# Kernel tuning notes

Measured on AMD Instinct MI355X. Metric: run time of the kernel, lower is better.

The kernel has to match this reference:

```python
import jax, jax.numpy as jnp
import numpy as np

NX, NU, N, BATCH = 64, 32, 32, 192
NEWTON_ITERS = 2  # fixed outer Newton iterations (original loops to kkt_tol)


def setup_inputs() -> dict:
    key = jax.random.key(0)
    ks = jax.random.split(key, 8)
    x0 = jax.random.normal(ks[0], (BATCH, NX), jnp.float32)
    x = 0.1 * jax.random.normal(ks[1], (N + 1, BATCH, NX), jnp.float32)
    u = 0.1 * jax.random.normal(ks[2], (N, BATCH, NU), jnp.float32)
    lmd = jnp.zeros((N + 1, BATCH, NX), jnp.float32)
    # linear dynamics x+ = A x + Bm u (stable-ish A)
    A = 0.9 * jnp.eye(NX, dtype=jnp.float32) + (0.1 / np.sqrt(NX)) * jax.random.normal(ks[3], (NX, NX), jnp.float32)
    Bm = jax.random.normal(ks[4], (NX, NU), jnp.float32) / np.sqrt(NX)
    # quadratic cost weights (symmetric PD)
    Cx = jax.random.normal(ks[5], (NX, NX), jnp.float32) / np.sqrt(NX)
    Qx = Cx @ Cx.T + 0.1 * jnp.eye(NX, dtype=jnp.float32)
    Cu = jax.random.normal(ks[6], (NU, NU), jnp.float32) / np.sqrt(NU)
    Ru = Cu @ Cu.T + jnp.eye(NU, dtype=jnp.float32)
    Cf = jax.random.normal(ks[7], (NX, NX), jnp.float32) / np.sqrt(NX)
    Qf = Cf @ Cf.T + 0.1 * jnp.eye(NX, dtype=jnp.float32)
    return {"x0": x0, "x": x, "u": u, "lmd": lmd, "A": A, "Bm": Bm, "Qx": Qx, "Ru": Ru, "Qf": Qf}


def _eval_kkt(x0, x, u, lmd, A, Bm, Qx, Ru, Qf):
    # KKT residuals of the LQ OCP (GaussNewton; vectorized over stages s and batch b)
    x0res = x[0] - x0                                                   # [B,nx]
    xs = x[:-1]                                                         # [N,B,nx]
    xres = jnp.einsum('ij,sbj->sbi', A, xs) + jnp.einsum('ij,sbj->sbi', Bm, u) - x[1:]
    lx = jnp.einsum('ij,sbj->sbi', Qx, xs) + jnp.einsum('ji,sbj->sbi', A, lmd[1:]) - lmd[:-1]
    lu = jnp.einsum('ij,sbj->sbi', Ru, u) + jnp.einsum('ji,sbj->sbi', Bm, lmd[1:])
    lxN = jnp.einsum('ij,bj->bi', Qf, x[-1]) - lmd[-1]                  # terminal gradient residual
    return x0res, xres, lx, lu, lxN


def _riccati(x0res, xres, lx, lu, lxN, A, Bm, Qx, Ru, Qf):
    B_, nx = x0res.shape
    PN = jnp.broadcast_to(Qf, (B_, nx, nx))

    def bwd(carry, inp):
        P, p = carry
        lx_i, lu_i, xres_i = inp
        PA = jnp.einsum('bij,jk->bik', P, A)
        PB = jnp.einsum('bij,jk->bik', P, Bm)
        Qxx = Qx[None] + jnp.einsum('ji,bjk->bik', A, PA)
        Quu = Ru[None] + jnp.einsum('ji,bjk->bik', Bm, PB)
        Qxu = jnp.einsum('ji,bjk->bik', A, PB)
        w = jnp.einsum('bij,bj->bi', P, xres_i) + p
        qx = lx_i + jnp.einsum('ji,bj->bi', A, w)
        qu = lu_i + jnp.einsum('ji,bj->bi', Bm, w)
        rhs = jnp.concatenate([jnp.swapaxes(Qxu, 1, 2), qu[..., None]], axis=2)
        sol = -jnp.linalg.solve(Quu, rhs)
        K, k = sol[..., :nx], sol[..., nx]
        Pn = Qxx + jnp.einsum('bxi,biy->bxy', Qxu, K)
        Pn = 0.5 * (Pn + jnp.swapaxes(Pn, 1, 2))
        pn = qx + jnp.einsum('bxi,bi->bx', Qxu, k)
        return (Pn, pn), (Pn, pn, K, k)

    (_, _), (Ps, ps, Ks, ks) = jax.lax.scan(bwd, (PN, lxN), (lx, lu, xres), reverse=True)
    Ps = jnp.concatenate([Ps, PN[None]], axis=0)   # [N+1,B,nx,nx]
    ps = jnp.concatenate([ps, lxN[None]], axis=0)  # [N+1,B,nx]

    def fwd(dx, inp):
        K, k, xres_i = inp
        du = jnp.einsum('bux,bx->bu', K, dx) + k
        dxn = jnp.einsum('ij,bj->bi', A, dx) + jnp.einsum('ij,bj->bi', Bm, du) + xres_i
        return dxn, (dx, du)

    dxN, (dxs, dus) = jax.lax.scan(fwd, -x0res, (Ks, ks, xres))
    dxs = jnp.concatenate([dxs, dxN[None]], axis=0)
    dlmd = jnp.einsum('sbij,sbj->sbi', Ps, dxs) + ps
    return dxs, dus, dlmd


def _solve(x0, x, u, lmd, A, Bm, Qx, Ru, Qf):
    for _ in range(NEWTON_ITERS):
        x0res, xres, lx, lu, lxN = _eval_kkt(x0, x, u, lmd, A, Bm, Qx, Ru, Qf)
        dx, du, dlmd = _riccati(x0res, xres, lx, lu, lxN, A, Bm, Qx, Ru, Qf)
        x = x + dx
        u = u + du
        lmd = lmd + dlmd
    return x, u, lmd


def reference(x0, x, u, lmd, A, Bm, Qx, Ru, Qf):
    # returns the optimized control trajectory u* [N,B,nu]
    return _solve(x0, x, u, lmd, A, Bm, Qx, Ru, Qf)[1]
```

## Files before the change

kernel.cpp:

```cpp
#include <hip/hip_runtime.h>

#define DEV __device__ __forceinline__

constexpr int NX = 64, NU = 32, NH = 32, NB = 192;

constexpr int WS_P  = 0;
constexpr int WS_QI = WS_P  + (NH + 1) * NX * NX;
constexpr int WS_XT = WS_QI + NH * NU * NU;
constexpr int WS_K  = WS_XT + NH * NU * NX;

typedef __attribute__((ext_vector_type(8))) short bf16x8;
typedef __attribute__((ext_vector_type(4))) float f32x4;
typedef __attribute__((ext_vector_type(4))) unsigned short us4;

constexpr int oM2Th = 0;
constexpr int oM2Tl = 13824;
constexpr int oPh   = 27648;
constexpr int oPl   = 36864;
constexpr int oTTh  = 46080;
constexpr int oTTl  = 59904;
constexpr int oXUh  = 73728;
constexpr int oXUl  = 78848;
constexpr int oKTh  = 83968;
constexpr int oKTl  = 89088;
constexpr int oQIh  = 94208;
constexpr int oQIl  = 96768;
constexpr int oQXX  = 99328;
constexpr int oQUU  = 116736;
constexpr int SMEMB = 121344;

DEV unsigned short bfh(float x) {
  unsigned u = __float_as_uint(x);
  return (unsigned short)((u + 0x7FFFu + ((u >> 16) & 1u)) >> 16);
}
DEV float bf2f(unsigned short h) { return __uint_as_float(((unsigned)h) << 16); }
DEV bf16x8 ldf(const char* base, int byteoff) { return *(const bf16x8*)(base + byteoff); }
DEV void st_pack4(char* hb, char* lb, int elemoff, f32x4 v) {
  us4 h, l;
#pragma unroll
  for (int r = 0; r < 4; ++r) {
    unsigned short hh = bfh(v[r]);
    h[r] = (short)hh;
    l[r] = (short)bfh(v[r] - bf2f(hh));
  }
  *(us4*)(hb + elemoff * 2) = h;
  *(us4*)(lb + elemoff * 2) = l;
}

DEV float4 ld4(const float* p) { return *reinterpret_cast<const float4*>(p); }
DEV void   st4(float* p, float4 v) { *reinterpret_cast<float4*>(p) = v; }
DEV float  dot4(float4 a, float4 b) {
  return fmaf(a.x, b.x, fmaf(a.y, b.y, fmaf(a.z, b.z, a.w * b.w)));
}
DEV void fma4(float4& a, float s, float4 b) {
  a.x = fmaf(s, b.x, a.x); a.y = fmaf(s, b.y, a.y);
  a.z = fmaf(s, b.z, a.z); a.w = fmaf(s, b.w, a.w);
}
DEV void fma8(float* acc, float s, float4 b0, float4 b1) {
  acc[0] = fmaf(s, b0.x, acc[0]); acc[1] = fmaf(s, b0.y, acc[1]);
  acc[2] = fmaf(s, b0.z, acc[2]); acc[3] = fmaf(s, b0.w, acc[3]);
  acc[4] = fmaf(s, b1.x, acc[4]); acc[5] = fmaf(s, b1.y, acc[5]);
  acc[6] = fmaf(s, b1.z, acc[6]); acc[7] = fmaf(s, b1.w, acc[7]);
}

#define MFMA16(a, b, c) __builtin_amdgcn_mfma_f32_16x16x32_bf16(a, b, c, 0, 0, 0)

DEV void producer(char* smem, const float* Ag, const float* Bg,
                  const float* Qxg, const float* Rug, const float* Qfg,
                  float* ws) {
  const int t = threadIdx.x, lane = t & 63, wv = t >> 6;
  const int l15 = lane & 15, l4 = lane >> 4;

  char* M2Th = smem + oM2Th; char* M2Tl = smem + oM2Tl;
  char* Ph   = smem + oPh;   char* Pl   = smem + oPl;
  char* TTh  = smem + oTTh;  char* TTl  = smem + oTTl;
  char* XUh  = smem + oXUh;  char* XUl  = smem + oXUl;
  char* KTh  = smem + oKTh;  char* KTl  = smem + oKTl;
  char* QIh  = smem + oQIh;  char* QIl  = smem + oQIl;
  float* QXX = (float*)(smem + oQXX);
  float* QUU = (float*)(smem + oQUU);

  float* gP  = ws + WS_P;
  float* gQI = ws + WS_QI;
  float* gXT = ws + WS_XT;
  float* gK  = ws + WS_K;
  int* flags = (int*)(ws + WS_P);

  for (int idx = t; idx < 96 * 64; idx += 512) {
    const int j = idx >> 6, m = idx & 63;
    const float v = (j < 64) ? Ag[m * 64 + j] : Bg[m * 32 + (j - 64)];
    const unsigned short h = bfh(v);
    *(unsigned short*)(M2Th + (j * 72 + m) * 2) = h;
    *(unsigned short*)(M2Tl + (j * 72 + m) * 2) = bfh(v - bf2f(h));
  }
  for (int idx = t; idx < 64 * 64; idx += 512) {
    const int r = idx >> 6, c = idx & 63;
    const float v = Qfg[idx];
    const unsigned short h = bfh(v);
    *(unsigned short*)(Ph + (r * 72 + c) * 2) = h;
    *(unsigned short*)(Pl + (r * 72 + c) * 2) = bfh(v - bf2f(h));
    gP[32 * 4096 + idx] = v;
  }
  __syncthreads();

  for (int s = NH - 1; s >= 0; --s) {
    for (int tt = wv; tt < 24; tt += 8) {
      const int mT = tt & 3, jT = tt >> 2;
      f32x4 acc = {0.f, 0.f, 0.f, 0.f};
#pragma unroll
      for (int kp = 0; kp < 2; ++kp) {
        const int ko = (kp * 32 + l4 * 8) * 2;
        const bf16x8 ah = ldf(Ph,   (mT * 16 + l15) * 144 + ko);
        const bf16x8 al = ldf(Pl,   (mT * 16 + l15) * 144 + ko);
        const bf16x8 bh = ldf(M2Th, (jT * 16 + l15) * 144 + ko);
        const bf16x8 bl = ldf(M2Tl, (jT * 16 + l15) * 144 + ko);
        acc = MFMA16(ah, bh, acc);
        acc = MFMA16(ah, bl, acc);
        acc = MFMA16(al, bh, acc);
      }
      st_pack4(TTh, TTl, (jT * 16 + l15) * 72 + mT * 16 + l4 * 4, acc);
    }
    __syncthreads();

    for (int tt = wv; tt < 36; tt += 8) {
      const int jT = tt / 6, iT = tt % 6;
      f32x4 acc = {0.f, 0.f, 0.f, 0.f};
#pragma unroll
      for (int kp = 0; kp < 2; ++kp) {
        const int ko = (kp * 32 + l4 * 8) * 2;
        const bf16x8 ah = ldf(TTh,  (jT * 16 + l15) * 144 + ko);
        const bf16x8 al = ldf(TTl,  (jT * 16 + l15) * 144 + ko);
        const bf16x8 bh = ldf(M2Th, (iT * 16 + l15) * 144 + ko);
        const bf16x8 bl = ldf(M2Tl, (iT * 16 + l15) * 144 + ko);
        acc = MFMA16(ah, bh, acc);
        acc = MFMA16(ah, bl, acc);
        acc = MFMA16(al, bh, acc);
      }
      const int c = iT * 16 + l15;
      const int j0 = jT * 16 + l4 * 4;
      if (jT < 4 && iT < 4) {
        const float4 q = ld4(Qxg + c * 64 + j0);
        float4 o; o.x = acc[0] + q.x; o.y = acc[1] + q.y;
        o.z = acc[2] + q.z; o.w = acc[3] + q.w;
        st4(QXX + c * 68 + j0, o);
      } else if (jT < 4) {
        const int n = c - 64;
        float4 o; o.x = acc[0]; o.y = acc[1]; o.z = acc[2]; o.w = acc[3];
        st4(gXT + s * 2048 + n * 64 + j0, o);
      } else if (iT < 4) {
        st_pack4(XUh, XUl, c * 40 + (j0 - 64), acc);
      } else {
        const int b = c - 64, a0 = j0 - 64;
        const float4 rv = ld4(Rug + b * 32 + a0);
        float4 o; o.x = acc[0] + rv.x; o.y = acc[1] + rv.y;
        o.z = acc[2] + rv.z; o.w = acc[3] + rv.w;
        st4(QUU + b * 36 + a0, o);
      }
    }
    __syncthreads();

    if (wv == 0) {
      const int i = lane & 31, h = lane >> 5;
      float W[16];
#pragma unroll
      for (int r = 0; r < 16; ++r) W[r] = QUU[i * 36 + h * 16 + r];
#pragma unroll
      for (int j = 0; j < 32; ++j) {
        const int jh = j >> 4, jr = j & 15;
        const float d = __shfl(W[jr], j | (jh << 5));
        const float pinv = 1.0f / d;
        const float f = __shfl(W[jr], i | (jh << 5));
        float pr[16];
#pragma unroll
        for (int r = 0; r < 16; ++r) pr[r] = __shfl(W[r], j | (h << 5));
        float nw[16];
        if (i == j) {
#pragma unroll
          for (int r = 0; r < 16; ++r) nw[r] = pr[r] * pinv;
          if (h == jh) nw[jr] = pinv;
        } else {
          const float g = f * pinv;
#pragma unroll
          for (int r = 0; r < 16; ++r) nw[r] = fmaf(-g, pr[r], W[r]);
          if (h == jh) nw[jr] = -g;
        }
#pragma unroll
        for (int r = 0; r < 16; ++r) W[r] = nw[r];
      }
#pragma unroll
      for (int q = 0; q < 4; ++q) {
        float4 o; o.x = W[4 * q]; o.y = W[4 * q + 1];
        o.z = W[4 * q + 2]; o.w = W[4 * q + 3];
        st4(gQI + s * 1024 + i * 32 + h * 16 + 4 * q, o);
        us4 hh, ll;
#pragma unroll
        for (int r = 0; r < 4; ++r) {
          const unsigned short hv = bfh(W[4 * q + r]);
          hh[r] = (short)hv;
          ll[r] = (short)bfh(W[4 * q + r] - bf2f(hv));
        }
        *(us4*)(QIh + (i * 40 + h * 16 + 4 * q) * 2) = hh;
        *(us4*)(QIl + (i * 40 + h * 16 + 4 * q) * 2) = ll;
      }
    }
    __syncthreads();

    {
      const int mT = wv & 1, xT = wv >> 1;
      f32x4 acc = {0.f, 0.f, 0.f, 0.f};
      const int ko = (l4 * 8) * 2;
      const bf16x8 ah = ldf(QIh, (mT * 16 + l15) * 80 + ko);
      const bf16x8 al = ldf(QIl, (mT * 16 + l15) * 80 + ko);
      const bf16x8 bh = ldf(XUh, (xT * 16 + l15) * 80 + ko);
      const bf16x8 bl = ldf(XUl, (xT * 16 + l15) * 80 + ko);
      acc = MFMA16(ah, bh, acc);
      acc = MFMA16(ah, bl, acc);
      acc = MFMA16(al, bh, acc);
      const int x = xT * 16 + l15, m0 = mT * 16 + l4 * 4;
#pragma unroll
      for (int r = 0; r < 4; ++r) gK[s * 2048 + (m0 + r) * 64 + x] = -acc[r];
      st_pack4(KTh, KTl, x * 40 + m0, acc);
    }
    __syncthreads();

    if (t == 0) {
      __threadfence();
      __hip_atomic_store(flags + s, 1, __ATOMIC_RELEASE, __HIP_MEMORY_SCOPE_AGENT);
    }

    if (s > 0) {
      for (int tt = wv; tt < 16; tt += 8) {
        const int iT = tt & 3, jT = tt >> 2;
        f32x4 acc = {0.f, 0.f, 0.f, 0.f};
        const int ko = (l4 * 8) * 2;
        const bf16x8 ah = ldf(XUh, (iT * 16 + l15) * 80 + ko);
        const bf16x8 al = ldf(XUl, (iT * 16 + l15) * 80 + ko);
        const bf16x8 bh = ldf(KTh, (jT * 16 + l15) * 80 + ko);
        const bf16x8 bl = ldf(KTl, (jT * 16 + l15) * 80 + ko);
        acc = MFMA16(ah, bh, acc);
        acc = MFMA16(ah, bl, acc);
        acc = MFMA16(al, bh, acc);
        const int j = jT * 16 + l15, i0 = iT * 16 + l4 * 4;
        f32x4 pv;
#pragma unroll
        for (int r = 0; r < 4; ++r) {
          pv[r] = QXX[(i0 + r) * 68 + j] - acc[r];
          gP[s * 4096 + (i0 + r) * 64 + j] = pv[r];
        }
        st_pack4(Ph, Pl, j * 72 + i0, pv);
      }
    }
    __syncthreads();
  }
}

DEV void consumer(float* lds, int b, const float* x0g, const float* xg,
                  const float* ug, const float* lg, const float* Ag,
                  const float* Bg, const float* Qxg, const float* Rug,
                  const float* Qfg, float* ws, float* outp) {
  const int t = threadIdx.x;
  const float* gP  = ws + WS_P;
  const float* gQI = ws + WS_QI;
  const float* gXT = ws + WS_XT;
  const float* gK  = ws + WS_K;
  const int* flags = (const int*)(ws + WS_P);

  float* sx   = lds;
  float* sl   = lds + 2112;
  float* su   = lds + 4224;
  float* sAT  = lds;
  float* xres = lds + 5248;
  float* lxs  = lds + 7296;
  float* lus  = lds + 9344;
  float* kv   = lds + 10368;
  float* swv  = lds + 11392;
  float* sqv  = lds + 11456;
  float* sduv = lds + 11488;
  float* sdxv = lds + 11520;

  for (int idx = t; idx < (NH + 1) * NX; idx += 512) {
    const int s = idx >> 6, i = idx & 63;
    sx[idx] = xg[(s * NB + b) * NX + i];
    sl[idx] = lg[(s * NB + b) * NX + i];
  }
  for (int idx = t; idx < NH * NU; idx += 512) {
    const int s = idx >> 5, j = idx & 31;
    su[idx] = ug[(s * NB + b) * NU + j];
  }
  __syncthreads();

  if (t < 256) {
    const int s = t >> 3, i0 = (t & 7) * 8;
    float accx[8], accl[8];
#pragma unroll
    for (int ii = 0; ii < 8; ++ii) {
      accx[ii] = -sx[(s + 1) * NX + i0 + ii];
      accl[ii] = -sl[s * NX + i0 + ii];
    }
#pragma unroll 2
    for (int k0 = 0; k0 < NX; k0 += 4) {
      const float4 xv = ld4(sx + s * NX + k0);
#pragma unroll
      for (int ii = 0; ii < 8; ++ii) {
        accx[ii] += dot4(ld4(Ag + (i0 + ii) * NX + k0), xv);
        accl[ii] += dot4(ld4(Qxg + (i0 + ii) * NX + k0), xv);
      }
    }
#pragma unroll 2
    for (int k0 = 0; k0 < NU; k0 += 4) {
      const float4 uv = ld4(su + s * NU + k0);
#pragma unroll
      for (int ii = 0; ii < 8; ++ii)
        accx[ii] += dot4(ld4(Bg + (i0 + ii) * NU + k0), uv);
    }
#pragma unroll 4
    for (int k = 0; k < NX; ++k) {
      const float lv = sl[(s + 1) * NX + k];
      fma8(accl, lv, ld4(Ag + k * NX + i0), ld4(Ag + k * NX + i0 + 4));
    }
#pragma unroll
    for (int ii = 0; ii < 8; ++ii) {
      xres[s * NX + i0 + ii] = accx[ii];
      lxs[s * NX + i0 + ii] = accl[ii];
    }
  }
  if (t < 256) {
    const int s = t >> 3, j0 = (t & 7) * 4;
    float4 acc = {0, 0, 0, 0};
#pragma unroll 2
    for (int k0 = 0; k0 < NU; k0 += 4) {
      const float4 uv = ld4(su + s * NU + k0);
      acc.x += dot4(ld4(Rug + (j0 + 0) * NU + k0), uv);
      acc.y += dot4(ld4(Rug + (j0 + 1) * NU + k0), uv);
      acc.z += dot4(ld4(Rug + (j0 + 2) * NU + k0), uv);
      acc.w += dot4(ld4(Rug + (j0 + 3) * NU + k0), uv);
    }
#pragma unroll 4
    for (int k = 0; k < NX; ++k) {
      const float lv = sl[(s + 1) * NX + k];
      fma4(acc, lv, ld4(Bg + k * NU + j0));
    }
    lus[s * NU + j0 + 0] = acc.x; lus[s * NU + j0 + 1] = acc.y;
    lus[s * NU + j0 + 2] = acc.z; lus[s * NU + j0 + 3] = acc.w;
  }

  float p_i = 0.0f, dx_i = 0.0f;
  if (t < 64) {
    const int i = t;
    float acc = -sl[NH * NX + i];
#pragma unroll 4
    for (int k0 = 0; k0 < NX; k0 += 4)
      acc += dot4(ld4(Qfg + i * NX + k0), ld4(sx + NH * NX + k0));
    p_i = acc;
    dx_i = x0g[b * NX + i] - sx[i];
  }
  __syncthreads();

  for (int idx = t; idx < NX * NX / 4; idx += 512) {
    const int k = idx >> 4, i4 = (idx & 15) * 4;
    const float4 a4 = ld4(Ag + k * NX + i4);
    sAT[(i4 + 0) * 68 + k] = a4.x;
    sAT[(i4 + 1) * 68 + k] = a4.y;
    sAT[(i4 + 2) * 68 + k] = a4.z;
    sAT[(i4 + 3) * 68 + k] = a4.w;
  }
  __syncthreads();

  if (t >= 64) return;

  const int i = t;
  const int j = t & 31;
  const int hh = t >> 5;

  for (int s = NH - 1; s >= 0; --s) {
    while (__hip_atomic_load(flags + s, __ATOMIC_ACQUIRE, __HIP_MEMORY_SCOPE_AGENT) == 0)
      __builtin_amdgcn_s_sleep(16);

    const float* Pr = gP + (s + 1) * NX * NX + i * NX;
    const float* xr = xres + s * NX;
    float w = p_i;
#pragma unroll
    for (int k0 = 0; k0 < NX; k0 += 16) {
      w += dot4(ld4(Pr + k0),      ld4(xr + k0));
      w += dot4(ld4(Pr + k0 + 4),  ld4(xr + k0 + 4));
      w += dot4(ld4(Pr + k0 + 8),  ld4(xr + k0 + 8));
      w += dot4(ld4(Pr + k0 + 12), ld4(xr + k0 + 12));
    }
    swv[i] = w;

    float qx = lxs[s * NX + i];
#pragma unroll
    for (int k0 = 0; k0 < NX; k0 += 16) {
      qx += dot4(ld4(sAT + i * 68 + k0),      ld4(swv + k0));
      qx += dot4(ld4(sAT + i * 68 + k0 + 4),  ld4(swv + k0 + 4));
      qx += dot4(ld4(sAT + i * 68 + k0 + 8),  ld4(swv + k0 + 8));
      qx += dot4(ld4(sAT + i * 68 + k0 + 12), ld4(swv + k0 + 12));
    }

    float qa = 0.0f;
    const int kb = hh * 32;
#pragma unroll 8
    for (int kk = 0; kk < 32; ++kk)
      qa = fmaf(Bg[(kb + kk) * NU + j], swv[kb + kk], qa);
    qa += __shfl_xor(qa, 32);
    const float qu = qa + lus[s * NU + j];
    if (hh == 0) sqv[j] = qu;

    const float* Qr = gQI + s * NU * NU + j * NU + hh * 16;
    float ka = dot4(ld4(Qr),      ld4(sqv + hh * 16))
             + dot4(ld4(Qr + 4),  ld4(sqv + hh * 16 + 4))
             + dot4(ld4(Qr + 8),  ld4(sqv + hh * 16 + 8))
             + dot4(ld4(Qr + 12), ld4(sqv + hh * 16 + 12));
    ka += __shfl_xor(ka, 32);
    if (hh == 0) kv[s * NU + j] = -ka;

    const float* Xs = gXT + s * NU * NX;
    float pp = qx;
#pragma unroll 8
    for (int m = 0; m < NU; ++m)
      pp = fmaf(Xs[m * NX + i], kv[s * NU + m], pp);
    p_i = pp;
  }

  sdxv[i] = dx_i;
  for (int s = 0; s < NH; ++s) {
    const float* Kr = gK + s * NU * NX + j * NX + hh * 32;
    const float* dxh = sdxv + hh * 32;
    float da = 0.0f;
#pragma unroll
    for (int k0 = 0; k0 < 32; k0 += 16) {
      da += dot4(ld4(Kr + k0),      ld4(dxh + k0));
      da += dot4(ld4(Kr + k0 + 4),  ld4(dxh + k0 + 4));
      da += dot4(ld4(Kr + k0 + 8),  ld4(dxh + k0 + 8));
      da += dot4(ld4(Kr + k0 + 12), ld4(dxh + k0 + 12));
    }
    da += __shfl_xor(da, 32);
    const float du = da + kv[s * NU + j];
    if (hh == 0) {
      const int gi = (s * NB + b) * NU + j;
      outp[gi] = ug[gi] + du;
      sduv[j] = du;
    }

    float nxv = xres[s * NX + i];
    const float* Ar = Ag + i * NX;
#pragma unroll
    for (int k0 = 0; k0 < NX; k0 += 4)
      nxv += dot4(ld4(Ar + k0), ld4(sdxv + k0));
    const float* Br = Bg + i * NU;
#pragma unroll
    for (int m0 = 0; m0 < NU; m0 += 4)
      nxv += dot4(ld4(Br + m0), ld4(sduv + m0));
    sdxv[i] = nxv;
  }
}

__global__ void k_zero(float* ws) {
  if (threadIdx.x < 64) ((int*)(ws + WS_P))[threadIdx.x] = 0;
}

__global__ __launch_bounds__(512) void k_fused(
    const float* __restrict__ x0g, const float* __restrict__ xg,
    const float* __restrict__ ug, const float* __restrict__ lg,
    const float* __restrict__ Ag, const float* __restrict__ Bg,
    const float* __restrict__ Qxg, const float* __restrict__ Rug,
    const float* __restrict__ Qfg, float* __restrict__ ws,
    float* __restrict__ outp) {
  __shared__ __align__(16) char smem[SMEMB];
  if (blockIdx.x == 0)
    producer(smem, Ag, Bg, Qxg, Rug, Qfg, ws);
  else
    consumer((float*)smem, blockIdx.x - 1, x0g, xg, ug, lg, Ag, Bg, Qxg, Rug,
             Qfg, ws, outp);
}

extern "C" void kernel_launch(void* const* d_in, const int* in_sizes, int n_in,
                              void* d_out, int out_size, void* d_ws, size_t ws_size,
                              hipStream_t stream) {
  const float* x0  = (const float*)d_in[0];
  const float* x   = (const float*)d_in[1];
  const float* u   = (const float*)d_in[2];
  const float* lmd = (const float*)d_in[3];
  const float* A   = (const float*)d_in[4];
  const float* Bm  = (const float*)d_in[5];
  const float* Qx  = (const float*)d_in[6];
  const float* Ru  = (const float*)d_in[7];
  const float* Qf  = (const float*)d_in[8];
  float* ws  = (float*)d_ws;
  float* out = (float*)d_out;

  hipLaunchKernelGGL(k_zero, dim3(1), dim3(64), 0, stream, ws);
  hipLaunchKernelGGL(k_fused, dim3(NB + 1), dim3(512), 0, stream,
                     x0, x, u, lmd, A, Bm, Qx, Ru, Qf, ws, out);
}
```

Before: 449.8 us.

## Restructure producer Riccati stages with 3-way bf16 split and overlapped GEMMs

The producer workgroup's per-stage Riccati pipeline is reorganized. The P*M2 product for the next stage now runs concurrently with the Quu inversion and Qxx computation, and only the needed blocks of M2^T(PM2) are computed. The bf16 splitting moves from two levels to three (hi/mid/lo, six MFMAs per block) for P, M2 and TT, which raises accuracy at the cost of more MFMA work. Global writebacks become nontemporal and the X block is stored transposed so the consumer can read it with vector dot4 loads. The consumer's flag spin now uses relaxed loads with a shorter sleep and a single acquire load afterwards.

Result: faster. 386.7 us (-14.0%).

```diff
diff --git a/kernel.cpp b/kernel.cpp
--- a/kernel.cpp
+++ b/kernel.cpp
@@ -6,49 +6,43 @@
 
 constexpr int WS_P  = 0;
 constexpr int WS_QI = WS_P  + (NH + 1) * NX * NX;
-constexpr int WS_XT = WS_QI + NH * NU * NU;
-constexpr int WS_K  = WS_XT + NH * NU * NX;
+constexpr int WS_X  = WS_QI + NH * NU * NU;
+constexpr int WS_K  = WS_X  + NH * NX * NU;
 
 typedef __attribute__((ext_vector_type(8))) short bf16x8;
 typedef __attribute__((ext_vector_type(4))) float f32x4;
 typedef __attribute__((ext_vector_type(4))) unsigned short us4;
 
-constexpr int oM2Th = 0;
-constexpr int oM2Tl = 13824;
-constexpr int oPh   = 27648;
-constexpr int oPl   = 36864;
-constexpr int oTTh  = 46080;
-constexpr int oTTl  = 59904;
-constexpr int oXUh  = 73728;
-constexpr int oXUl  = 78848;
-constexpr int oKTh  = 83968;
-constexpr int oKTl  = 89088;
-constexpr int oQIh  = 94208;
-constexpr int oQIl  = 96768;
-constexpr int oQXX  = 99328;
-constexpr int oQUU  = 116736;
-constexpr int SMEMB = 121344;
+constexpr int LVL_M2T = 96 * 72 * 2;
+constexpr int LVL_P   = 64 * 72 * 2;
+constexpr int LVL_TT  = 96 * 72 * 2;
+constexpr int LVL_XU  = 64 * 40 * 2;
+constexpr int LVL_KT  = 64 * 40 * 2;
+constexpr int LVL_QI  = 32 * 40 * 2;
+constexpr int oM2T = 0;
+constexpr int oP   = oM2T + 3 * LVL_M2T;
+constexpr int oTT  = oP   + 3 * LVL_P;
+constexpr int oXU  = oTT  + 3 * LVL_TT;
+constexpr int oKT  = oXU  + 2 * LVL_XU;
+constexpr int oQI  = oKT  + 2 * LVL_KT;
+constexpr int oQXX = oQI  + 2 * LVL_QI;
+constexpr int SMEMB = oQXX + 64 * 68 * 4;
 
 DEV unsigned short bfh(float x) {
   unsigned u = __float_as_uint(x);
   return (unsigned short)((u + 0x7FFFu + ((u >> 16) & 1u)) >> 16);
 }
 DEV float bf2f(unsigned short h) { return __uint_as_float(((unsigned)h) << 16); }
-DEV bf16x8 ldf(const char* base, int byteoff) { return *(const bf16x8*)(base + byteoff); }
-DEV void st_pack4(char* hb, char* lb, int elemoff, f32x4 v) {
-  us4 h, l;
-#pragma unroll
-  for (int r = 0; r < 4; ++r) {
-    unsigned short hh = bfh(v[r]);
-    h[r] = (short)hh;
-    l[r] = (short)bfh(v[r] - bf2f(hh));
-  }
-  *(us4*)(hb + elemoff * 2) = h;
-  *(us4*)(lb + elemoff * 2) = l;
-}
-
+DEV void split3(float x, unsigned short& h, unsigned short& m, unsigned short& l) {
+  h = bfh(x); float r1 = x - bf2f(h);
+  m = bfh(r1); float r2 = r1 - bf2f(m);
+  l = bfh(r2);
+}
 DEV float4 ld4(const float* p) { return *reinterpret_cast<const float4*>(p); }
 DEV void   st4(float* p, float4 v) { *reinterpret_cast<float4*>(p) = v; }
+DEV void st4_nt(float* p, f32x4 v) {
+  __builtin_nontemporal_store(v, (f32x4*)p);
+}
 DEV float  dot4(float4 a, float4 b) {
   return fmaf(a.x, b.x, fmaf(a.y, b.y, fmaf(a.z, b.z, a.w * b.w)));
 }
@@ -65,96 +59,140 @@
 
 #define MFMA16(a, b, c) __builtin_amdgcn_mfma_f32_16x16x32_bf16(a, b, c, 0, 0, 0)
 
+DEV f32x4 prod33(const char* A, int ao, int LA, const char* B, int bo, int LB,
+                 f32x4 acc) {
+  const bf16x8 a0 = *(const bf16x8*)(A + ao);
+  const bf16x8 a1 = *(const bf16x8*)(A + LA + ao);
+  const bf16x8 a2 = *(const bf16x8*)(A + 2 * LA + ao);
+  const bf16x8 b0 = *(const bf16x8*)(B + bo);
+  const bf16x8 b1 = *(const bf16x8*)(B + LB + bo);
+  const bf16x8 b2 = *(const bf16x8*)(B + 2 * LB + bo);
+  acc = MFMA16(a1, b1, acc);
+  acc = MFMA16(a2, b0, acc);
+  acc = MFMA16(a0, b2, acc);
+  acc = MFMA16(a1, b0, acc);
+  acc = MFMA16(a0, b1, acc);
+  acc = MFMA16(a0, b0, acc);
+  return acc;
+}
+DEV f32x4 prod22(const char* A, int ao, int LA, const char* B, int bo, int LB,
+                 f32x4 acc) {
+  const bf16x8 a0 = *(const bf16x8*)(A + ao);
+  const bf16x8 a1 = *(const bf16x8*)(A + LA + ao);
+  const bf16x8 b0 = *(const bf16x8*)(B + bo);
+  const bf16x8 b1 = *(const bf16x8*)(B + LB + bo);
+  acc = MFMA16(a1, b0, acc);
+  acc = MFMA16(a0, b1, acc);
+  acc = MFMA16(a0, b0, acc);
+  return acc;
+}
+DEV void st_pack3(char* base, int lvl, int el, f32x4 v) {
+  us4 h, m, l;
+#pragma unroll
+  for (int r = 0; r < 4; ++r) {
+    unsigned short hh, mm, ll; split3(v[r], hh, mm, ll);
+    h[r] = (short)hh; m[r] = (short)mm; l[r] = (short)ll;
+  }
+  *(us4*)(base + el * 2) = h;
+  *(us4*)(base + lvl + el * 2) = m;
+  *(us4*)(base + 2 * lvl + el * 2) = l;
+}
+DEV void st_pack2(char* base, int lvl, int el, f32x4 v) {
+  us4 h, l;
+#pragma unroll
+  for (int r = 0; r < 4; ++r) {
+    const unsigned short hh = bfh(v[r]);
+    h[r] = (short)hh;
+    l[r] = (short)bfh(v[r] - bf2f(hh));
+  }
+  *(us4*)(base + el * 2) = h;
+  *(us4*)(base + lvl + el * 2) = l;
+}
+
 DEV void producer(char* smem, const float* Ag, const float* Bg,
                   const float* Qxg, const float* Rug, const float* Qfg,
                   float* ws) {
   const int t = threadIdx.x, lane = t & 63, wv = t >> 6;
   const int l15 = lane & 15, l4 = lane >> 4;
 
-  char* M2Th = smem + oM2Th; char* M2Tl = smem + oM2Tl;
-  char* Ph   = smem + oPh;   char* Pl   = smem + oPl;
-  char* TTh  = smem + oTTh;  char* TTl  = smem + oTTl;
-  char* XUh  = smem + oXUh;  char* XUl  = smem + oXUl;
-  char* KTh  = smem + oKTh;  char* KTl  = smem + oKTl;
-  char* QIh  = smem + oQIh;  char* QIl  = smem + oQIl;
+  char* M2T = smem + oM2T;
+  char* Pp  = smem + oP;
+  char* TT  = smem + oTT;
+  char* XU  = smem + oXU;
+  char* KT  = smem + oKT;
+  char* QI  = smem + oQI;
   float* QXX = (float*)(smem + oQXX);
-  float* QUU = (float*)(smem + oQUU);
+  float* QUU = (float*)(smem + oQXX);
 
   float* gP  = ws + WS_P;
   float* gQI = ws + WS_QI;
-  float* gXT = ws + WS_XT;
+  float* gX  = ws + WS_X;
   float* gK  = ws + WS_K;
   int* flags = (int*)(ws + WS_P);
 
   for (int idx = t; idx < 96 * 64; idx += 512) {
     const int j = idx >> 6, m = idx & 63;
     const float v = (j < 64) ? Ag[m * 64 + j] : Bg[m * 32 + (j - 64)];
-    const unsigned short h = bfh(v);
-    *(unsigned short*)(M2Th + (j * 72 + m) * 2) = h;
-    *(unsigned short*)(M2Tl + (j * 72 + m) * 2) = bfh(v - bf2f(h));
+    unsigned short h, mi, lo; split3(v, h, mi, lo);
+    const int eo = (j * 72 + m) * 2;
+    *(unsigned short*)(M2T + eo) = h;
+    *(unsigned short*)(M2T + LVL_M2T + eo) = mi;
+    *(unsigned short*)(M2T + 2 * LVL_M2T + eo) = lo;
   }
   for (int idx = t; idx < 64 * 64; idx += 512) {
     const int r = idx >> 6, c = idx & 63;
     const float v = Qfg[idx];
-    const unsigned short h = bfh(v);
-    *(unsigned short*)(Ph + (r * 72 + c) * 2) = h;
-    *(unsigned short*)(Pl + (r * 72 + c) * 2) = bfh(v - bf2f(h));
-    gP[32 * 4096 + idx] = v;
+    unsigned short h, mi, lo; split3(v, h, mi, lo);
+    const int eo = (r * 72 + c) * 2;
+    *(unsigned short*)(Pp + eo) = h;
+    *(unsigned short*)(Pp + LVL_P + eo) = mi;
+    *(unsigned short*)(Pp + 2 * LVL_P + eo) = lo;
+    __builtin_nontemporal_store(v, gP + 32 * 4096 + idx);
   }
   __syncthreads();
 
   for (int s = NH - 1; s >= 0; --s) {
-    for (int tt = wv; tt < 24; tt += 8) {
-      const int mT = tt & 3, jT = tt >> 2;
+    {
+      const int mT = wv >> 1, jT = 4 + (wv & 1);
       f32x4 acc = {0.f, 0.f, 0.f, 0.f};
 #pragma unroll
       for (int kp = 0; kp < 2; ++kp) {
-        const int ko = (kp * 32 + l4 * 8) * 2;
-        const bf16x8 ah = ldf(Ph,   (mT * 16 + l15) * 144 + ko);
-        const bf16x8 al = ldf(Pl,   (mT * 16 + l15) * 144 + ko);
-        const bf16x8 bh = ldf(M2Th, (jT * 16 + l15) * 144 + ko);
-        const bf16x8 bl = ldf(M2Tl, (jT * 16 + l15) * 144 + ko);
-        acc = MFMA16(ah, bh, acc);
-        acc = MFMA16(ah, bl, acc);
-        acc = MFMA16(al, bh, acc);
-      }
-      st_pack4(TTh, TTl, (jT * 16 + l15) * 72 + mT * 16 + l4 * 4, acc);
+        const int ao = ((mT * 16 + l15) * 72 + kp * 32 + l4 * 8) * 2;
+        const int bo = ((jT * 16 + l15) * 72 + kp * 32 + l4 * 8) * 2;
+        acc = prod33(Pp, ao, LVL_P, M2T, bo, LVL_M2T, acc);
+      }
+      st_pack3(TT, LVL_TT, (jT * 16 + l15) * 72 + mT * 16 + l4 * 4, acc);
     }
     __syncthreads();
 
-    for (int tt = wv; tt < 36; tt += 8) {
-      const int jT = tt / 6, iT = tt % 6;
+    if (wv < 4) {
+      const int uA = wv >> 1, uB = wv & 1;
       f32x4 acc = {0.f, 0.f, 0.f, 0.f};
 #pragma unroll
       for (int kp = 0; kp < 2; ++kp) {
-        const int ko = (kp * 32 + l4 * 8) * 2;
-        const bf16x8 ah = ldf(TTh,  (jT * 16 + l15) * 144 + ko);
-        const bf16x8 al = ldf(TTl,  (jT * 16 + l15) * 144 + ko);
-        const bf16x8 bh = ldf(M2Th, (iT * 16 + l15) * 144 + ko);
-        const bf16x8 bl = ldf(M2Tl, (iT * 16 + l15) * 144 + ko);
-        acc = MFMA16(ah, bh, acc);
-        acc = MFMA16(ah, bl, acc);
-        acc = MFMA16(al, bh, acc);
-      }
-      const int c = iT * 16 + l15;
-      const int j0 = jT * 16 + l4 * 4;
-      if (jT < 4 && iT < 4) {
-        const float4 q = ld4(Qxg + c * 64 + j0);
-        float4 o; o.x = acc[0] + q.x; o.y = acc[1] + q.y;
-        o.z = acc[2] + q.z; o.w = acc[3] + q.w;
-        st4(QXX + c * 68 + j0, o);
-      } else if (jT < 4) {
-        const int n = c - 64;
-        float4 o; o.x = acc[0]; o.y = acc[1]; o.z = acc[2]; o.w = acc[3];
-        st4(gXT + s * 2048 + n * 64 + j0, o);
-      } else if (iT < 4) {
-        st_pack4(XUh, XUl, c * 40 + (j0 - 64), acc);
-      } else {
-        const int b = c - 64, a0 = j0 - 64;
-        const float4 rv = ld4(Rug + b * 32 + a0);
-        float4 o; o.x = acc[0] + rv.x; o.y = acc[1] + rv.y;
-        o.z = acc[2] + rv.z; o.w = acc[3] + rv.w;
-        st4(QUU + b * 36 + a0, o);
+        const int ao = (((4 + uA) * 16 + l15) * 72 + kp * 32 + l4 * 8) * 2;
+        const int bo = ((64 + uB * 16 + l15) * 72 + kp * 32 + l4 * 8) * 2;
+        acc = prod33(TT, ao, LVL_TT, M2T, bo, LVL_M2T, acc);
+      }
+      const int c = uB * 16 + l15, u0 = uA * 16 + l4 * 4;
+      const float4 rv = ld4(Rug + c * 32 + u0);
+      QUU[c * 36 + u0 + 0] = acc[0] + rv.x;
+      QUU[c * 36 + u0 + 1] = acc[1] + rv.y;
+      QUU[c * 36 + u0 + 2] = acc[2] + rv.z;
+      QUU[c * 36 + u0 + 3] = acc[3] + rv.w;
+    } else {
+      for (int q = wv - 4; q < 8; q += 4) {
+        const int uT = q & 1, xT = q >> 1;
+        f32x4 acc = {0.f, 0.f, 0.f, 0.f};
+#pragma unroll
+        for (int kp = 0; kp < 2; ++kp) {
+          const int ao = (((4 + uT) * 16 + l15) * 72 + kp * 32 + l4 * 8) * 2;
+          const int bo = ((xT * 16 + l15) * 72 + kp * 32 + l4 * 8) * 2;
+          acc = prod33(TT, ao, LVL_TT, M2T, bo, LVL_M2T, acc);
+        }
+        const int x = xT * 16 + l15, u0 = uT * 16 + l4 * 4;
+        st_pack2(XU, LVL_XU, x * 40 + u0, acc);
+        st4_nt(gX + s * 2048 + x * 32 + u0, acc);
       }
     }
     __syncthreads();
@@ -189,9 +227,8 @@
       }
 #pragma unroll
       for (int q = 0; q < 4; ++q) {
-        float4 o; o.x = W[4 * q]; o.y = W[4 * q + 1];
-        o.z = W[4 * q + 2]; o.w = W[4 * q + 3];
-        st4(gQI + s * 1024 + i * 32 + h * 16 + 4 * q, o);
+        f32x4 o = {W[4 * q], W[4 * q + 1], W[4 * q + 2], W[4 * q + 3]};
+        st4_nt(gQI + s * 1024 + i * 32 + h * 16 + 4 * q, o);
         us4 hh, ll;
 #pragma unroll
         for (int r = 0; r < 4; ++r) {
@@ -199,27 +236,54 @@
           hh[r] = (short)hv;
           ll[r] = (short)bfh(W[4 * q + r] - bf2f(hv));
         }
-        *(us4*)(QIh + (i * 40 + h * 16 + 4 * q) * 2) = hh;
-        *(us4*)(QIl + (i * 40 + h * 16 + 4 * q) * 2) = ll;
+        *(us4*)(QI + (i * 40 + h * 16 + 4 * q) * 2) = hh;
+        *(us4*)(QI + LVL_QI + (i * 40 + h * 16 + 4 * q) * 2) = ll;
+      }
+    } else {
+      for (int tt = wv - 1; tt < 16; tt += 7) {
+        const int mT = tt & 3, jT = tt >> 2;
+        f32x4 acc = {0.f, 0.f, 0.f, 0.f};
+#pragma unroll
+        for (int kp = 0; kp < 2; ++kp) {
+          const int ao = ((mT * 16 + l15) * 72 + kp * 32 + l4 * 8) * 2;
+          const int bo = ((jT * 16 + l15) * 72 + kp * 32 + l4 * 8) * 2;
+          acc = prod33(Pp, ao, LVL_P, M2T, bo, LVL_M2T, acc);
+        }
+        st_pack3(TT, LVL_TT, (jT * 16 + l15) * 72 + mT * 16 + l4 * 4, acc);
       }
     }
     __syncthreads();
 
-    {
-      const int mT = wv & 1, xT = wv >> 1;
-      f32x4 acc = {0.f, 0.f, 0.f, 0.f};
-      const int ko = (l4 * 8) * 2;
-      const bf16x8 ah = ldf(QIh, (mT * 16 + l15) * 80 + ko);
-      const bf16x8 al = ldf(QIl, (mT * 16 + l15) * 80 + ko);
-      const bf16x8 bh = ldf(XUh, (xT * 16 + l15) * 80 + ko);
-      const bf16x8 bl = ldf(XUl, (xT * 16 + l15) * 80 + ko);
-      acc = MFMA16(ah, bh, acc);
-      acc = MFMA16(ah, bl, acc);
-      acc = MFMA16(al, bh, acc);
-      const int x = xT * 16 + l15, m0 = mT * 16 + l4 * 4;
-#pragma unroll
-      for (int r = 0; r < 4; ++r) gK[s * 2048 + (m0 + r) * 64 + x] = -acc[r];
-      st_pack4(KTh, KTl, x * 40 + m0, acc);
+    if (wv < 2) {
+      for (int tt = wv; tt < 8; tt += 2) {
+        const int mT = tt & 1, xT = tt >> 1;
+        f32x4 acc = {0.f, 0.f, 0.f, 0.f};
+        const int ao = ((mT * 16 + l15) * 40 + l4 * 8) * 2;
+        const int bo = ((xT * 16 + l15) * 40 + l4 * 8) * 2;
+        acc = prod22(QI, ao, LVL_QI, XU, bo, LVL_XU, acc);
+        const int x = xT * 16 + l15, m0 = mT * 16 + l4 * 4;
+#pragma unroll
+        for (int r = 0; r < 4; ++r)
+          __builtin_nontemporal_store(-acc[r], gK + s * 2048 + (m0 + r) * 64 + x);
+        st_pack2(KT, LVL_KT, x * 40 + m0, acc);
+      }
+    } else {
+      for (int tt = wv - 2; tt < 16; tt += 6) {
+        const int jT = tt >> 2, iT = tt & 3;
+        f32x4 acc = {0.f, 0.f, 0.f, 0.f};
+#pragma unroll
+        for (int kp = 0; kp < 2; ++kp) {
+          const int ao = ((jT * 16 + l15) * 72 + kp * 32 + l4 * 8) * 2;
+          const int bo = ((iT * 16 + l15) * 72 + kp * 32 + l4 * 8) * 2;
+          acc = prod33(TT, ao, LVL_TT, M2T, bo, LVL_M2T, acc);
+        }
+        const int c = iT * 16 + l15, j0 = jT * 16 + l4 * 4;
+        const float4 q = ld4(Qxg + c * 64 + j0);
+        QXX[c * 68 + j0 + 0] = acc[0] + q.x;
+        QXX[c * 68 + j0 + 1] = acc[1] + q.y;
+        QXX[c * 68 + j0 + 2] = acc[2] + q.z;
+        QXX[c * 68 + j0 + 3] = acc[3] + q.w;
+      }
     }
     __syncthreads();
 
@@ -232,22 +296,17 @@
       for (int tt = wv; tt < 16; tt += 8) {
         const int iT = tt & 3, jT = tt >> 2;
         f32x4 acc = {0.f, 0.f, 0.f, 0.f};
-        const int ko = (l4 * 8) * 2;
-        const bf16x8 ah = ldf(XUh, (iT * 16 + l15) * 80 + ko);
-        const bf16x8 al = ldf(XUl, (iT * 16 + l15) * 80 + ko);
-        const bf16x8 bh = ldf(KTh, (jT * 16 + l15) * 80 + ko);
-        const bf16x8 bl = ldf(KTl, (jT * 16 + l15) * 80 + ko);
-        acc = MFMA16(ah, bh, acc);
-        acc = MFMA16(ah, bl, acc);
-        acc = MFMA16(al, bh, acc);
+        const int ao = ((iT * 16 + l15) * 40 + l4 * 8) * 2;
+        const int bo = ((jT * 16 + l15) * 40 + l4 * 8) * 2;
+        acc = prod22(XU, ao, LVL_XU, KT, bo, LVL_KT, acc);
         const int j = jT * 16 + l15, i0 = iT * 16 + l4 * 4;
         f32x4 pv;
 #pragma unroll
         for (int r = 0; r < 4; ++r) {
           pv[r] = QXX[(i0 + r) * 68 + j] - acc[r];
-          gP[s * 4096 + (i0 + r) * 64 + j] = pv[r];
+          __builtin_nontemporal_store(pv[r], gP + s * 4096 + (i0 + r) * 64 + j);
         }
-        st_pack4(Ph, Pl, j * 72 + i0, pv);
+        st_pack3(Pp, LVL_P, j * 72 + i0, pv);
       }
     }
     __syncthreads();
@@ -261,9 +320,9 @@
   const int t = threadIdx.x;
   const float* gP  = ws + WS_P;
   const float* gQI = ws + WS_QI;
-  const float* gXT = ws + WS_XT;
+  const float* gX  = ws + WS_X;
   const float* gK  = ws + WS_K;
-  const int* flags = (const int*)(ws + WS_P);
+  int* flags = (int*)(ws + WS_P);
 
   float* sx   = lds;
   float* sl   = lds + 2112;
@@ -373,8 +432,11 @@
   const int hh = t >> 5;
 
   for (int s = NH - 1; s >= 0; --s) {
-    while (__hip_atomic_load(flags + s, __ATOMIC_ACQUIRE, __HIP_MEMORY_SCOPE_AGENT) == 0)
-      __builtin_amdgcn_s_sleep(16);
+    while (__hip_atomic_load(flags + s, __ATOMIC_RELAXED,
+                             __HIP_MEMORY_SCOPE_AGENT) == 0)
+      __builtin_amdgcn_s_sleep(4);
+    (void)__hip_atomic_load(flags + s, __ATOMIC_ACQUIRE,
+                            __HIP_MEMORY_SCOPE_AGENT);
 
     const float* Pr = gP + (s + 1) * NX * NX + i * NX;
     const float* xr = xres + s * NX;
@@ -414,11 +476,11 @@
     ka += __shfl_xor(ka, 32);
     if (hh == 0) kv[s * NU + j] = -ka;
 
-    const float* Xs = gXT + s * NU * NX;
+    const float* Xs = gX + s * 2048 + i * 32;
     float pp = qx;
-#pragma unroll 8
-    for (int m = 0; m < NU; ++m)
-      pp = fmaf(Xs[m * NX + i], kv[s * NU + m], pp);
+#pragma unroll
+    for (int m0 = 0; m0 < NU; m0 += 4)
+      pp += dot4(ld4(Xs + m0), ld4(kv + s * NU + m0));
     p_i = pp;
   }
 
```
